# Optimization experiments

Hardware: AMD Instinct MI355X
Metric: run time of the kernel (lower is better)

Reference implementation:

```python
import jax, jax.numpy as jnp
import numpy as np

STRIDE = 1
PAD = 1
DIL = 1


def setup_inputs() -> dict:
    key = jax.random.key(0)
    k1, k2, k3, k4 = jax.random.split(key, 4)
    N, Cin, H, W = 4, 256, 64, 64
    Cout, kh, kw = 256, 3, 3
    inputs = jax.random.normal(k1, (N, Cin, H, W), jnp.float32)
    filter = jax.random.normal(k2, (Cout, Cin, kh, kw), jnp.float32) * 0.05
    # offsets in pixels (y,x interleaved per tap), typical magnitude O(1)
    offset = jax.random.normal(k3, (N, 2 * kh * kw, H, W), jnp.float32)
    # modulation mask in [0,1) (post-sigmoid in real nets)
    mask = jax.random.uniform(k4, (N, kh * kw, H, W), jnp.float32)
    return {"inputs": inputs, "filter": filter, "offset": offset, "mask": mask}


def _dcn_forward(inputs, filt, offset, mask):
    N, C, H, W = inputs.shape
    Cout, _, kh, kw = filt.shape
    K = kh * kw
    Ho = (H + 2 * PAD - DIL * (kh - 1) - 1) // STRIDE + 1
    Wo = (W + 2 * PAD - DIL * (kw - 1) - 1) // STRIDE + 1

    # base sampling grid per kernel tap: [K, Ho, Wo]
    ki, kj = jnp.meshgrid(jnp.arange(kh), jnp.arange(kw), indexing='ij')
    ki = ki.reshape(K, 1, 1)
    kj = kj.reshape(K, 1, 1)
    base_y = (jnp.arange(Ho)[None, :, None] * STRIDE - PAD + ki * DIL).astype(jnp.float32)
    base_x = (jnp.arange(Wo)[None, None, :] * STRIDE - PAD + kj * DIL).astype(jnp.float32)

    # offset channels: per tap k, channel 2k = dy, channel 2k+1 = dx
    off = offset.reshape(N, K, 2, Ho, Wo)
    y = base_y[None] + off[:, :, 0]  # [N, K, Ho, Wo]
    x = base_x[None] + off[:, :, 1]

    y0 = jnp.floor(y)
    x0 = jnp.floor(x)
    ly = y - y0  # fractional parts, [N, K, Ho, Wo]
    lx = x - x0
    y0i = y0.astype(jnp.int32)
    x0i = x0.astype(jnp.int32)

    def gather(img, yy, xx):
        # img [C,H,W]; yy,xx [K,Ho,Wo] int; zero outside bounds
        valid = (yy >= 0) & (yy < H) & (xx >= 0) & (xx < W)
        yc = jnp.clip(yy, 0, H - 1)
        xc = jnp.clip(xx, 0, W - 1)
        return img[:, yc, xc] * valid.astype(img.dtype)  # [C,K,Ho,Wo]

    def sample_one(img, y0i, x0i, ly, lx):
        v00 = gather(img, y0i, x0i)
        v01 = gather(img, y0i, x0i + 1)
        v10 = gather(img, y0i + 1, x0i)
        v11 = gather(img, y0i + 1, x0i + 1)
        return (v00 * (1 - ly) * (1 - lx) + v01 * (1 - ly) * lx
                + v10 * ly * (1 - lx) + v11 * ly * lx)

    # bilinear-sampled, modulated im2col columns: [N, C, K, Ho, Wo]
    col = jax.vmap(sample_one)(inputs, y0i, x0i, ly, lx)
    col = col * mask.reshape(N, 1, K, Ho, Wo)

    # grouped conv with num_groups=1: plain GEMM over (C, K)
    out = jnp.einsum('ock,nckhw->nohw', filt.reshape(Cout, C, K), col)
    return out


def reference(inputs, filter, offset, mask):
    return _dcn_forward(inputs, filter, offset, mask)
```

## Files before the change

kernel.cpp:

```cpp
#include <hip/hip_runtime.h>
#include <stdint.h>

typedef __attribute__((ext_vector_type(4))) float f32x4;
typedef __attribute__((ext_vector_type(8))) short bf16x8;

static constexpr int N_ = 4, C_ = 256, HW_ = 4096;
static constexpr int CO_ = 256, KTAP = 9, KK = 2304;
static constexpr int NSTEP = 72;
static constexpr int A_STEP_BYTES = 16 * 64 * 16;

static constexpr size_t NHWC_BYTES = (size_t)N_ * HW_ * C_ * 2;
static constexpr size_t ABF_OFF    = NHWC_BYTES;
static constexpr size_t ABF_BYTES  = (size_t)NSTEP * A_STEP_BYTES;

__device__ inline unsigned f2bf(float f) {
  unsigned u = __builtin_bit_cast(unsigned, f);
  unsigned r = u + 0x7FFFu + ((u >> 16) & 1u);
  return r >> 16;
}
__device__ inline float asf(unsigned u) { return __builtin_bit_cast(float, u); }

__global__ __launch_bounds__(256) void k_nchw_to_nhwc(const float* __restrict__ in,
                                                      unsigned short* __restrict__ nhwc) {
  __shared__ float tile[64][65];
  int b = blockIdx.x;
  int n = b >> 8, cg = (b >> 6) & 3, hwg = b & 63;
  int c0 = cg * 64, hw0 = hwg * 64;
  int t = threadIdx.x;
  int col = t & 63, r0 = t >> 6;
  const float* src = in + (size_t)(n * C_ + c0) * HW_ + hw0;
#pragma unroll
  for (int i = 0; i < 16; ++i) {
    int row = r0 + i * 4;
    tile[row][col] = src[(size_t)row * HW_ + col];
  }
  __syncthreads();
  int pr = t >> 2, cc0 = (t & 3) * 16;
  unsigned us[8];
#pragma unroll
  for (int i = 0; i < 8; ++i) {
    unsigned lo = f2bf(tile[cc0 + 2 * i][pr]);
    unsigned hi = f2bf(tile[cc0 + 2 * i + 1][pr]);
    us[i] = lo | (hi << 16);
  }
  unsigned* dst = (unsigned*)(nhwc + (size_t)(n * HW_ + hw0 + pr) * C_ + c0 + cc0);
  ((uint4*)dst)[0] = make_uint4(us[0], us[1], us[2], us[3]);
  ((uint4*)dst)[1] = make_uint4(us[4], us[5], us[6], us[7]);
}

__global__ __launch_bounds__(256) void k_prep_filter(const float* __restrict__ filt,
                                                     unsigned short* __restrict__ abf2) {
  int gid = blockIdx.x * 256 + threadIdx.x;
  int o = gid >> 8, c = gid & 255;
  const float* f = filt + (size_t)(o * C_ + c) * KTAP;
  int rb = o >> 4;
  int lane = ((c >> 3) & 3) * 16 + (o & 15);
  int j = c & 7;
#pragma unroll
  for (int tap = 0; tap < KTAP; ++tap) {
    int s = tap * 8 + (c >> 5);
    abf2[((size_t)(s * 16 + rb) * 64 + lane) * 8 + j] = (unsigned short)f2bf(f[tap]);
  }
}

__device__ __forceinline__ void buildB(const uint2* g, f32x4 w, unsigned short* dst) {
  float r0 = w.x * asf(g[0].x << 16) + w.y * asf(g[1].x << 16) +
             w.z * asf(g[2].x << 16) + w.w * asf(g[3].x << 16);
  float r1 = w.x * asf(g[0].x & 0xffff0000u) + w.y * asf(g[1].x & 0xffff0000u) +
             w.z * asf(g[2].x & 0xffff0000u) + w.w * asf(g[3].x & 0xffff0000u);
  float r2 = w.x * asf(g[0].y << 16) + w.y * asf(g[1].y << 16) +
             w.z * asf(g[2].y << 16) + w.w * asf(g[3].y << 16);
  float r3 = w.x * asf(g[0].y & 0xffff0000u) + w.y * asf(g[1].y & 0xffff0000u) +
             w.z * asf(g[2].y & 0xffff0000u) + w.w * asf(g[3].y & 0xffff0000u);
  *(uint2*)dst = make_uint2(f2bf(r0) | (f2bf(r1) << 16), f2bf(r2) | (f2bf(r3) << 16));
}

#define MFMA_BF16 __builtin_amdgcn_mfma_f32_16x16x32_bf16

#define PIPE_STEP(S, GCON, WCON, GISS, WISS, AC0, AC1, AN0, AN1, RDP, WRP)            \
  do {                                                                                \
    int s1_ = (S) + 1; if (s1_ >= NSTEP) s1_ = NSTEP - 1;                             \
    int s2_ = (S) + 2; if (s2_ >= NSTEP) s2_ = NSTEP - 1;                             \
    AN0 = *(const bf16x8*)(aoff0 + (size_t)s1_ * A_STEP_BYTES);                       \
    AN1 = *(const bf16x8*)(aoff1 + (size_t)s1_ * A_STEP_BYTES);                       \
    if ((s2_ & 7) == 0) {                                                             \
      int tp_ = s2_ >> 3;                                                             \
      raS = *(const uint4*)&recA[(tp_ * 64 + p_b) * 4];                               \
      wS  = *(const f32x4*)&recW[(tp_ * 64 + p_b) * 4];                               \
    }                                                                                 \
    {                                                                                 \
      unsigned sc_ = (unsigned)((s2_ & 7) * 64);                                      \
      GISS[0] = *(const uint2*)(nb_t + raS.x + sc_);                                  \
      GISS[1] = *(const uint2*)(nb_t + raS.y + sc_);                                  \
      GISS[2] = *(const uint2*)(nb_t + raS.z + sc_);                                  \
      GISS[3] = *(const uint2*)(nb_t + raS.w + sc_);                                  \
    }                                                                                 \
    WISS = wS;                                                                        \
    __builtin_amdgcn_sched_barrier(0);                                                \
    {                                                                                 \
      const char* bb_ = (const char*)&Bl[RDP][0] + boff;                              \
      bf16x8 b0_ = *(const bf16x8*)(bb_);                                             \
      bf16x8 b1_ = *(const bf16x8*)(bb_ + 1280);                                      \
      bf16x8 b2_ = *(const bf16x8*)(bb_ + 2560);                                      \
      bf16x8 b3_ = *(const bf16x8*)(bb_ + 3840);                                      \
      __builtin_amdgcn_s_setprio(1);                                                  \
      acc[0][0] = MFMA_BF16(AC0, b0_, acc[0][0], 0, 0, 0);                            \
      acc[1][0] = MFMA_BF16(AC1, b0_, acc[1][0], 0, 0, 0);                            \
      acc[0][1] = MFMA_BF16(AC0, b1_, acc[0][1], 0, 0, 0);                            \
      acc[1][1] = MFMA_BF16(AC1, b1_, acc[1][1], 0, 0, 0);                            \
      acc[0][2] = MFMA_BF16(AC0, b2_, acc[0][2], 0, 0, 0);                            \
      acc[1][2] = MFMA_BF16(AC1, b2_, acc[1][2], 0, 0, 0);                            \
      acc[0][3] = MFMA_BF16(AC0, b3_, acc[0][3], 0, 0, 0);                            \
      acc[1][3] = MFMA_BF16(AC1, b3_, acc[1][3], 0, 0, 0);                            \
      __builtin_amdgcn_s_setprio(0);                                                  \
    }                                                                                 \
    buildB(GCON, WCON, (WRP) ? bw1 : bw0);                                            \
    asm volatile("s_waitcnt lgkmcnt(0)" ::: "memory");                                \
    __builtin_amdgcn_s_barrier();                                                     \
    asm volatile("" ::: "memory");                                                    \
  } while (0)

__global__ __launch_bounds__(512, 2) void k_dcn_gemm(const unsigned short* __restrict__ nhwc,
                                                     const unsigned short* __restrict__ abf2,
                                                     const float* __restrict__ offs,
                                                     const float* __restrict__ msk,
                                                     float* __restrict__ out) {
  __shared__ __align__(16) unsigned short Bl[2][64 * 40];
  __shared__ float recW[KTAP * 64 * 4];
  __shared__ unsigned recA[KTAP * 64 * 4];

  int bid = blockIdx.x;
  int b = ((bid & 7) << 5) | (bid >> 3);
  int n = b >> 6;
  int ho = b & 63;
  int hw0 = ho << 6;
  int t = threadIdx.x;

  for (int r = t; r < 576; r += 512) {
    int pl = r / 9;
    int tap = r - pl * 9;
    int hw = hw0 + pl;
    float dy = offs[(size_t)(n * 18 + 2 * tap) * HW_ + hw];
    float dx = offs[(size_t)(n * 18 + 2 * tap + 1) * HW_ + hw];
    float mk = msk[(size_t)(n * 9 + tap) * HW_ + hw];
    float y = (float)(ho - 1 + tap / 3) + dy;
    float x = (float)(pl - 1 + tap % 3) + dx;
    float fy = floorf(y), fx = floorf(x);
    float ly = y - fy, lx = x - fx;
    int y0 = (int)fy, x0 = (int)fx;
    int y1 = y0 + 1, x1 = x0 + 1;
    float vy0 = (y0 >= 0 && y0 < 64) ? 1.f : 0.f;
    float vy1 = (y1 >= 0 && y1 < 64) ? 1.f : 0.f;
    float vx0 = (x0 >= 0 && x0 < 64) ? 1.f : 0.f;
    float vx1 = (x1 >= 0 && x1 < 64) ? 1.f : 0.f;
    int y0c = min(max(y0, 0), 63), y1c = min(max(y1, 0), 63);
    int x0c = min(max(x0, 0), 63), x1c = min(max(x1, 0), 63);
    int base = (tap * 64 + pl) * 4;
    recW[base + 0] = (1.f - ly) * (1.f - lx) * mk * vy0 * vx0;
    recW[base + 1] = (1.f - ly) * lx * mk * vy0 * vx1;
    recW[base + 2] = ly * (1.f - lx) * mk * vy1 * vx0;
    recW[base + 3] = ly * lx * mk * vy1 * vx1;
    recA[base + 0] = (unsigned)((y0c * 64 + x0c) * 512);
    recA[base + 1] = (unsigned)((y0c * 64 + x1c) * 512);
    recA[base + 2] = (unsigned)((y1c * 64 + x0c) * 512);
    recA[base + 3] = (unsigned)((y1c * 64 + x1c) * 512);
  }
  __syncthreads();

  int lane = t & 63, wv = t >> 6;
  int p_b = t >> 3, cg = t & 7;

  const char* aoff0 = (const char*)abf2 + ((wv * 2 + 0) * 64 + lane) * 16;
  const char* aoff1 = (const char*)abf2 + ((wv * 2 + 1) * 64 + lane) * 16;
  const char* nb_t = (const char*)nhwc + (size_t)n * HW_ * C_ * 2 + cg * 8;
  unsigned short* bw0 = &Bl[0][p_b * 40 + cg * 4];
  unsigned short* bw1 = &Bl[1][p_b * 40 + cg * 4];
  const int boff = ((lane & 15) * 40 + (lane >> 4) * 8) * 2;

  f32x4 acc[2][4];
#pragma unroll
  for (int mi = 0; mi < 2; ++mi)
#pragma unroll
    for (int ni = 0; ni < 4; ++ni) acc[mi][ni] = (f32x4){0.f, 0.f, 0.f, 0.f};

  uint2 gA[4], gB[4];
  f32x4 wA, wB, wS;
  uint4 raS;

  raS = *(const uint4*)&recA[p_b * 4];
  wS  = *(const f32x4*)&recW[p_b * 4];
  gA[0] = *(const uint2*)(nb_t + raS.x);
  gA[1] = *(const uint2*)(nb_t + raS.y);
  gA[2] = *(const uint2*)(nb_t + raS.z);
  gA[3] = *(const uint2*)(nb_t + raS.w);
  wA = wS;
  gB[0] = *(const uint2*)(nb_t + raS.x + 64);
  gB[1] = *(const uint2*)(nb_t + raS.y + 64);
  gB[2] = *(const uint2*)(nb_t + raS.z + 64);
  gB[3] = *(const uint2*)(nb_t + raS.w + 64);
  wB = wS;
  bf16x8 afc0 = *(const bf16x8*)(aoff0);
  bf16x8 afc1 = *(const bf16x8*)(aoff1);
  bf16x8 afn0, afn1;

  buildB(gA, wA, bw0);
  asm volatile("s_waitcnt lgkmcnt(0)" ::: "memory");
  __builtin_amdgcn_s_barrier();
  asm volatile("" ::: "memory");

  for (int s = 0; s < NSTEP; s += 2) {
    PIPE_STEP(s,     gB, wB, gA, wA, afc0, afc1, afn0, afn1, 0, 1);
    PIPE_STEP(s + 1, gA, wA, gB, wB, afn0, afn1, afc0, afc1, 1, 0);
  }

  float* ob = out + (size_t)n * CO_ * HW_ + hw0;
#pragma unroll
  for (int mi = 0; mi < 2; ++mi)
#pragma unroll
    for (int ni = 0; ni < 4; ++ni)
#pragma unroll
      for (int j = 0; j < 4; ++j) {
        int o = wv * 32 + mi * 16 + (lane >> 4) * 4 + j;
        int hw = ni * 16 + (lane & 15);
        ob[(size_t)o * HW_ + hw] = acc[mi][ni][j];
      }
}

extern "C" void kernel_launch(void* const* d_in, const int* in_sizes, int n_in,
                              void* d_out, int out_size, void* d_ws, size_t ws_size,
                              hipStream_t stream) {
  const float* inp  = (const float*)d_in[0];
  const float* filt = (const float*)d_in[1];
  const float* offs = (const float*)d_in[2];
  const float* msk  = (const float*)d_in[3];
  float* out = (float*)d_out;
  if (ws_size < ABF_OFF + ABF_BYTES) return;
  unsigned short* nhwc = (unsigned short*)d_ws;
  unsigned short* abf2 = (unsigned short*)((char*)d_ws + ABF_OFF);

  k_nchw_to_nhwc<<<1024, 256, 0, stream>>>(inp, nhwc);
  k_prep_filter<<<256, 256, 0, stream>>>(filt, abf2);
  k_dcn_gemm<<<256, 512, 0, stream>>>(nhwc, abf2, offs, msk, out);
}
```

Baseline: 56.35 us.

## Process two K-steps per barrier phase with a swizzled-free LDS B layout

```diff
diff --git a/kernel.cpp b/kernel.cpp
--- a/kernel.cpp
+++ b/kernel.cpp
@@ -63,7 +63,10 @@
   }
 }
 
-__device__ __forceinline__ void buildB(const uint2* g, f32x4 w, unsigned short* dst) {
+struct GBank { uint2 g[8]; f32x4 w; };
+struct AFrags { bf16x8 f[4]; };
+
+__device__ __forceinline__ void buildB4(const uint2* g, f32x4 w, char* dst) {
   float r0 = w.x * asf(g[0].x << 16) + w.y * asf(g[1].x << 16) +
              w.z * asf(g[2].x << 16) + w.w * asf(g[3].x << 16);
   float r1 = w.x * asf(g[0].x & 0xffff0000u) + w.y * asf(g[1].x & 0xffff0000u) +
@@ -77,47 +80,68 @@
 
 #define MFMA_BF16 __builtin_amdgcn_mfma_f32_16x16x32_bf16
 
-#define PIPE_STEP(S, GCON, WCON, GISS, WISS, AC0, AC1, AN0, AN1, RDP, WRP)            \
-  do {                                                                                \
-    int s1_ = (S) + 1; if (s1_ >= NSTEP) s1_ = NSTEP - 1;                             \
-    int s2_ = (S) + 2; if (s2_ >= NSTEP) s2_ = NSTEP - 1;                             \
-    AN0 = *(const bf16x8*)(aoff0 + (size_t)s1_ * A_STEP_BYTES);                       \
-    AN1 = *(const bf16x8*)(aoff1 + (size_t)s1_ * A_STEP_BYTES);                       \
-    if ((s2_ & 7) == 0) {                                                             \
-      int tp_ = s2_ >> 3;                                                             \
-      raS = *(const uint4*)&recA[(tp_ * 64 + p_b) * 4];                               \
-      wS  = *(const f32x4*)&recW[(tp_ * 64 + p_b) * 4];                               \
-    }                                                                                 \
-    {                                                                                 \
-      unsigned sc_ = (unsigned)((s2_ & 7) * 64);                                      \
-      GISS[0] = *(const uint2*)(nb_t + raS.x + sc_);                                  \
-      GISS[1] = *(const uint2*)(nb_t + raS.y + sc_);                                  \
-      GISS[2] = *(const uint2*)(nb_t + raS.z + sc_);                                  \
-      GISS[3] = *(const uint2*)(nb_t + raS.w + sc_);                                  \
-    }                                                                                 \
-    WISS = wS;                                                                        \
-    __builtin_amdgcn_sched_barrier(0);                                                \
-    {                                                                                 \
-      const char* bb_ = (const char*)&Bl[RDP][0] + boff;                              \
-      bf16x8 b0_ = *(const bf16x8*)(bb_);                                             \
-      bf16x8 b1_ = *(const bf16x8*)(bb_ + 1280);                                      \
-      bf16x8 b2_ = *(const bf16x8*)(bb_ + 2560);                                      \
-      bf16x8 b3_ = *(const bf16x8*)(bb_ + 3840);                                      \
-      __builtin_amdgcn_s_setprio(1);                                                  \
-      acc[0][0] = MFMA_BF16(AC0, b0_, acc[0][0], 0, 0, 0);                            \
-      acc[1][0] = MFMA_BF16(AC1, b0_, acc[1][0], 0, 0, 0);                            \
-      acc[0][1] = MFMA_BF16(AC0, b1_, acc[0][1], 0, 0, 0);                            \
-      acc[1][1] = MFMA_BF16(AC1, b1_, acc[1][1], 0, 0, 0);                            \
-      acc[0][2] = MFMA_BF16(AC0, b2_, acc[0][2], 0, 0, 0);                            \
-      acc[1][2] = MFMA_BF16(AC1, b2_, acc[1][2], 0, 0, 0);                            \
-      acc[0][3] = MFMA_BF16(AC0, b3_, acc[0][3], 0, 0, 0);                            \
-      acc[1][3] = MFMA_BF16(AC1, b3_, acc[1][3], 0, 0, 0);                            \
-      __builtin_amdgcn_s_setprio(0);                                                  \
-    }                                                                                 \
-    buildB(GCON, WCON, (WRP) ? bw1 : bw0);                                            \
-    asm volatile("s_waitcnt lgkmcnt(0)" ::: "memory");                                \
-    __builtin_amdgcn_s_barrier();                                                     \
-    asm volatile("" ::: "memory");                                                    \
+#define PHASE(S, GC, GI, AC, AN, RDP, WRP)                                        \
+  do {                                                                            \
+    int sa_ = (S) + 2 < NSTEP ? (S) + 2 : NSTEP - 1;                              \
+    int sb_ = (S) + 3 < NSTEP ? (S) + 3 : NSTEP - 1;                              \
+    int s4_ = (S) + 4 < NSTEP ? (S) + 4 : NSTEP - 1;                              \
+    int s5_ = (S) + 5 < NSTEP ? (S) + 5 : NSTEP - 1;                              \
+    AN.f[0] = *(const bf16x8*)(aoff0 + (size_t)sa_ * A_STEP_BYTES);               \
+    AN.f[1] = *(const bf16x8*)(aoff1 + (size_t)sa_ * A_STEP_BYTES);               \
+    AN.f[2] = *(const bf16x8*)(aoff0 + (size_t)sb_ * A_STEP_BYTES);               \
+    AN.f[3] = *(const bf16x8*)(aoff1 + (size_t)sb_ * A_STEP_BYTES);               \
+    {                                                                             \
+      int tp_ = s4_ >> 3;                                                         \
+      uint4 ra_ = *(const uint4*)&recA[(tp_ * 64 + p_b) * 4];                     \
+      GI.w = *(const f32x4*)&recW[(tp_ * 64 + p_b) * 4];                          \
+      unsigned c4_ = (unsigned)((s4_ & 7) * 64);                                  \
+      unsigned c5_ = (unsigned)((s5_ & 7) * 64);                                  \
+      GI.g[0] = *(const uint2*)(nb_t + ra_.x + c4_);                              \
+      GI.g[1] = *(const uint2*)(nb_t + ra_.y + c4_);                              \
+      GI.g[2] = *(const uint2*)(nb_t + ra_.z + c4_);                              \
+      GI.g[3] = *(const uint2*)(nb_t + ra_.w + c4_);                              \
+      GI.g[4] = *(const uint2*)(nb_t + ra_.x + c5_);                              \
+      GI.g[5] = *(const uint2*)(nb_t + ra_.y + c5_);                              \
+      GI.g[6] = *(const uint2*)(nb_t + ra_.z + c5_);                              \
+      GI.g[7] = *(const uint2*)(nb_t + ra_.w + c5_);                              \
+    }                                                                             \
+    __builtin_amdgcn_sched_barrier(0);                                            \
+    {                                                                             \
+      const char* bb_ = (const char*)&Bl[0][0] + (RDP) * 8192 + boff;             \
+      bf16x8 b0_ = *(const bf16x8*)(bb_ + 0);                                     \
+      bf16x8 b1_ = *(const bf16x8*)(bb_ + 256);                                   \
+      bf16x8 b2_ = *(const bf16x8*)(bb_ + 512);                                   \
+      bf16x8 b3_ = *(const bf16x8*)(bb_ + 768);                                   \
+      __builtin_amdgcn_s_setprio(1);                                              \
+      acc[0][0] = MFMA_BF16(AC.f[0], b0_, acc[0][0], 0, 0, 0);                    \
+      acc[1][0] = MFMA_BF16(AC.f[1], b0_, acc[1][0], 0, 0, 0);                    \
+      acc[0][1] = MFMA_BF16(AC.f[0], b1_, acc[0][1], 0, 0, 0);                    \
+      acc[1][1] = MFMA_BF16(AC.f[1], b1_, acc[1][1], 0, 0, 0);                    \
+      acc[0][2] = MFMA_BF16(AC.f[0], b2_, acc[0][2], 0, 0, 0);                    \
+      acc[1][2] = MFMA_BF16(AC.f[1], b2_, acc[1][2], 0, 0, 0);                    \
+      acc[0][3] = MFMA_BF16(AC.f[0], b3_, acc[0][3], 0, 0, 0);                    \
+      acc[1][3] = MFMA_BF16(AC.f[1], b3_, acc[1][3], 0, 0, 0);                    \
+      __builtin_amdgcn_s_setprio(0);                                              \
+      bf16x8 b4_ = *(const bf16x8*)(bb_ + 4096 + 0);                              \
+      bf16x8 b5_ = *(const bf16x8*)(bb_ + 4096 + 256);                            \
+      bf16x8 b6_ = *(const bf16x8*)(bb_ + 4096 + 512);                            \
+      bf16x8 b7_ = *(const bf16x8*)(bb_ + 4096 + 768);                            \
+      __builtin_amdgcn_s_setprio(1);                                              \
+      acc[0][0] = MFMA_BF16(AC.f[2], b4_, acc[0][0], 0, 0, 0);                    \
+      acc[1][0] = MFMA_BF16(AC.f[3], b4_, acc[1][0], 0, 0, 0);                    \
+      acc[0][1] = MFMA_BF16(AC.f[2], b5_, acc[0][1], 0, 0, 0);                    \
+      acc[1][1] = MFMA_BF16(AC.f[3], b5_, acc[1][1], 0, 0, 0);                    \
+      acc[0][2] = MFMA_BF16(AC.f[2], b6_, acc[0][2], 0, 0, 0);                    \
+      acc[1][2] = MFMA_BF16(AC.f[3], b6_, acc[1][2], 0, 0, 0);                    \
+      acc[0][3] = MFMA_BF16(AC.f[2], b7_, acc[0][3], 0, 0, 0);                    \
+      acc[1][3] = MFMA_BF16(AC.f[3], b7_, acc[1][3], 0, 0, 0);                    \
+      __builtin_amdgcn_s_setprio(0);                                              \
+    }                                                                             \
+    buildB4(&GC.g[0], GC.w, bwp + (WRP) * 8192 + 0);                              \
+    buildB4(&GC.g[4], GC.w, bwp + (WRP) * 8192 + 4096);                           \
+    asm volatile("s_waitcnt lgkmcnt(0)" ::: "memory");                            \
+    __builtin_amdgcn_s_barrier();                                                 \
+    asm volatile("" ::: "memory");                                                \
   } while (0)
 
 __global__ __launch_bounds__(512, 2) void k_dcn_gemm(const unsigned short* __restrict__ nhwc,
@@ -125,7 +149,7 @@
                                                      const float* __restrict__ offs,
                                                      const float* __restrict__ msk,
                                                      float* __restrict__ out) {
-  __shared__ __align__(16) unsigned short Bl[2][64 * 40];
+  __shared__ __align__(16) unsigned short Bl[2][4096];
   __shared__ float recW[KTAP * 64 * 4];
   __shared__ unsigned recA[KTAP * 64 * 4];
 
@@ -173,9 +197,8 @@
   const char* aoff0 = (const char*)abf2 + ((wv * 2 + 0) * 64 + lane) * 16;
   const char* aoff1 = (const char*)abf2 + ((wv * 2 + 1) * 64 + lane) * 16;
   const char* nb_t = (const char*)nhwc + (size_t)n * HW_ * C_ * 2 + cg * 8;
-  unsigned short* bw0 = &Bl[0][p_b * 40 + cg * 4];
-  unsigned short* bw1 = &Bl[1][p_b * 40 + cg * 4];
-  const int boff = ((lane & 15) * 40 + (lane >> 4) * 8) * 2;
+  char* bwp = (char*)&Bl[0][0] + ((cg >> 1) * 1024 + p_b * 16 + (cg & 1) * 8);
+  const int boff = (lane >> 4) * 1024 + (lane & 15) * 16;
 
   f32x4 acc[2][4];
 #pragma unroll
@@ -183,34 +206,44 @@
 #pragma unroll
     for (int ni = 0; ni < 4; ++ni) acc[mi][ni] = (f32x4){0.f, 0.f, 0.f, 0.f};
 
-  uint2 gA[4], gB[4];
-  f32x4 wA, wB, wS;
-  uint4 raS;
-
-  raS = *(const uint4*)&recA[p_b * 4];
-  wS  = *(const f32x4*)&recW[p_b * 4];
-  gA[0] = *(const uint2*)(nb_t + raS.x);
-  gA[1] = *(const uint2*)(nb_t + raS.y);
-  gA[2] = *(const uint2*)(nb_t + raS.z);
-  gA[3] = *(const uint2*)(nb_t + raS.w);
-  wA = wS;
-  gB[0] = *(const uint2*)(nb_t + raS.x + 64);
-  gB[1] = *(const uint2*)(nb_t + raS.y + 64);
-  gB[2] = *(const uint2*)(nb_t + raS.z + 64);
-  gB[3] = *(const uint2*)(nb_t + raS.w + 64);
-  wB = wS;
-  bf16x8 afc0 = *(const bf16x8*)(aoff0);
-  bf16x8 afc1 = *(const bf16x8*)(aoff1);
-  bf16x8 afn0, afn1;
-
-  buildB(gA, wA, bw0);
-  asm volatile("s_waitcnt lgkmcnt(0)" ::: "memory");
-  __builtin_amdgcn_s_barrier();
-  asm volatile("" ::: "memory");
-
-  for (int s = 0; s < NSTEP; s += 2) {
-    PIPE_STEP(s,     gB, wB, gA, wA, afc0, afc1, afn0, afn1, 0, 1);
-    PIPE_STEP(s + 1, gA, wA, gB, wB, afn0, afn1, afc0, afc1, 1, 0);
+  GBank gA, gB;
+  AFrags aC, aN;
+
+  {
+    uint4 ra0 = *(const uint4*)&recA[p_b * 4];
+    f32x4 w0 = *(const f32x4*)&recW[p_b * 4];
+    gA.w = w0;
+    gB.w = w0;
+    gA.g[0] = *(const uint2*)(nb_t + ra0.x + 0);
+    gA.g[1] = *(const uint2*)(nb_t + ra0.y + 0);
+    gA.g[2] = *(const uint2*)(nb_t + ra0.z + 0);
+    gA.g[3] = *(const uint2*)(nb_t + ra0.w + 0);
+    gA.g[4] = *(const uint2*)(nb_t + ra0.x + 64);
+    gA.g[5] = *(const uint2*)(nb_t + ra0.y + 64);
+    gA.g[6] = *(const uint2*)(nb_t + ra0.z + 64);
+    gA.g[7] = *(const uint2*)(nb_t + ra0.w + 64);
+    gB.g[0] = *(const uint2*)(nb_t + ra0.x + 128);
+    gB.g[1] = *(const uint2*)(nb_t + ra0.y + 128);
+    gB.g[2] = *(const uint2*)(nb_t + ra0.z + 128);
+    gB.g[3] = *(const uint2*)(nb_t + ra0.w + 128);
+    gB.g[4] = *(const uint2*)(nb_t + ra0.x + 192);
+    gB.g[5] = *(const uint2*)(nb_t + ra0.y + 192);
+    gB.g[6] = *(const uint2*)(nb_t + ra0.z + 192);
+    gB.g[7] = *(const uint2*)(nb_t + ra0.w + 192);
+    aC.f[0] = *(const bf16x8*)(aoff0);
+    aC.f[1] = *(const bf16x8*)(aoff1);
+    aC.f[2] = *(const bf16x8*)(aoff0 + A_STEP_BYTES);
+    aC.f[3] = *(const bf16x8*)(aoff1 + A_STEP_BYTES);
+    buildB4(&gA.g[0], gA.w, bwp + 0);
+    buildB4(&gA.g[4], gA.w, bwp + 4096);
+    asm volatile("s_waitcnt lgkmcnt(0)" ::: "memory");
+    __builtin_amdgcn_s_barrier();
+    asm volatile("" ::: "memory");
+  }
+
+  for (int s = 0; s < NSTEP; s += 4) {
+    PHASE(s,     gB, gA, aC, aN, 0, 1);
+    PHASE(s + 2, gA, gB, aN, aC, 1, 0);
   }
 
   float* ob = out + (size_t)n * CO_ * HW_ + hw0;
```

Measured after the change: 59.78 us. +6.1%, slower.

## Double threads per block, halve per-wave work, swizzle B tile layout

Applied to the files above, without the earlier changes.

```diff
diff --git a/kernel.cpp b/kernel.cpp
--- a/kernel.cpp
+++ b/kernel.cpp
@@ -63,69 +63,62 @@
   }
 }
 
-__device__ __forceinline__ void buildB(const uint2* g, f32x4 w, unsigned short* dst) {
-  float r0 = w.x * asf(g[0].x << 16) + w.y * asf(g[1].x << 16) +
-             w.z * asf(g[2].x << 16) + w.w * asf(g[3].x << 16);
-  float r1 = w.x * asf(g[0].x & 0xffff0000u) + w.y * asf(g[1].x & 0xffff0000u) +
-             w.z * asf(g[2].x & 0xffff0000u) + w.w * asf(g[3].x & 0xffff0000u);
-  float r2 = w.x * asf(g[0].y << 16) + w.y * asf(g[1].y << 16) +
-             w.z * asf(g[2].y << 16) + w.w * asf(g[3].y << 16);
-  float r3 = w.x * asf(g[0].y & 0xffff0000u) + w.y * asf(g[1].y & 0xffff0000u) +
-             w.z * asf(g[2].y & 0xffff0000u) + w.w * asf(g[3].y & 0xffff0000u);
-  *(uint2*)dst = make_uint2(f2bf(r0) | (f2bf(r1) << 16), f2bf(r2) | (f2bf(r3) << 16));
+struct GB { unsigned g[4]; f32x4 w; };
+
+__device__ __forceinline__ void buildB2(const unsigned* g, f32x4 w, char* dst) {
+  float r0 = w.x * asf(g[0] << 16) + w.y * asf(g[1] << 16) +
+             w.z * asf(g[2] << 16) + w.w * asf(g[3] << 16);
+  float r1 = w.x * asf(g[0] & 0xffff0000u) + w.y * asf(g[1] & 0xffff0000u) +
+             w.z * asf(g[2] & 0xffff0000u) + w.w * asf(g[3] & 0xffff0000u);
+  *(unsigned*)dst = f2bf(r0) | (f2bf(r1) << 16);
 }
 
 #define MFMA_BF16 __builtin_amdgcn_mfma_f32_16x16x32_bf16
 
-#define PIPE_STEP(S, GCON, WCON, GISS, WISS, AC0, AC1, AN0, AN1, RDP, WRP)            \
-  do {                                                                                \
-    int s1_ = (S) + 1; if (s1_ >= NSTEP) s1_ = NSTEP - 1;                             \
-    int s2_ = (S) + 2; if (s2_ >= NSTEP) s2_ = NSTEP - 1;                             \
-    AN0 = *(const bf16x8*)(aoff0 + (size_t)s1_ * A_STEP_BYTES);                       \
-    AN1 = *(const bf16x8*)(aoff1 + (size_t)s1_ * A_STEP_BYTES);                       \
-    if ((s2_ & 7) == 0) {                                                             \
-      int tp_ = s2_ >> 3;                                                             \
-      raS = *(const uint4*)&recA[(tp_ * 64 + p_b) * 4];                               \
-      wS  = *(const f32x4*)&recW[(tp_ * 64 + p_b) * 4];                               \
-    }                                                                                 \
-    {                                                                                 \
-      unsigned sc_ = (unsigned)((s2_ & 7) * 64);                                      \
-      GISS[0] = *(const uint2*)(nb_t + raS.x + sc_);                                  \
-      GISS[1] = *(const uint2*)(nb_t + raS.y + sc_);                                  \
-      GISS[2] = *(const uint2*)(nb_t + raS.z + sc_);                                  \
-      GISS[3] = *(const uint2*)(nb_t + raS.w + sc_);                                  \
-    }                                                                                 \
-    WISS = wS;                                                                        \
-    __builtin_amdgcn_sched_barrier(0);                                                \
-    {                                                                                 \
-      const char* bb_ = (const char*)&Bl[RDP][0] + boff;                              \
-      bf16x8 b0_ = *(const bf16x8*)(bb_);                                             \
-      bf16x8 b1_ = *(const bf16x8*)(bb_ + 1280);                                      \
-      bf16x8 b2_ = *(const bf16x8*)(bb_ + 2560);                                      \
-      bf16x8 b3_ = *(const bf16x8*)(bb_ + 3840);                                      \
-      __builtin_amdgcn_s_setprio(1);                                                  \
-      acc[0][0] = MFMA_BF16(AC0, b0_, acc[0][0], 0, 0, 0);                            \
-      acc[1][0] = MFMA_BF16(AC1, b0_, acc[1][0], 0, 0, 0);                            \
-      acc[0][1] = MFMA_BF16(AC0, b1_, acc[0][1], 0, 0, 0);                            \
-      acc[1][1] = MFMA_BF16(AC1, b1_, acc[1][1], 0, 0, 0);                            \
-      acc[0][2] = MFMA_BF16(AC0, b2_, acc[0][2], 0, 0, 0);                            \
-      acc[1][2] = MFMA_BF16(AC1, b2_, acc[1][2], 0, 0, 0);                            \
-      acc[0][3] = MFMA_BF16(AC0, b3_, acc[0][3], 0, 0, 0);                            \
-      acc[1][3] = MFMA_BF16(AC1, b3_, acc[1][3], 0, 0, 0);                            \
-      __builtin_amdgcn_s_setprio(0);                                                  \
-    }                                                                                 \
-    buildB(GCON, WCON, (WRP) ? bw1 : bw0);                                            \
-    asm volatile("s_waitcnt lgkmcnt(0)" ::: "memory");                                \
-    __builtin_amdgcn_s_barrier();                                                     \
-    asm volatile("" ::: "memory");                                                    \
+#define PIPE(S, GCON, GISS, ACUR, ANXT, RDP, WRP)                                 \
+  do {                                                                            \
+    int s1_ = (S) + 1 < NSTEP ? (S) + 1 : NSTEP - 1;                              \
+    int s2_ = (S) + 2 < NSTEP ? (S) + 2 : NSTEP - 1;                              \
+    ANXT = *(const bf16x8*)(aoff + (size_t)s1_ * A_STEP_BYTES);                   \
+    if ((s2_ & 7) == 0) {                                                         \
+      int tp_ = s2_ >> 3;                                                         \
+      raS = *(const uint4*)&recA[(tp_ * 64 + p_b) * 4];                           \
+      wS  = *(const f32x4*)&recW[(tp_ * 64 + p_b) * 4];                           \
+    }                                                                             \
+    {                                                                             \
+      unsigned co_ = (unsigned)((s2_ & 7) * 64);                                  \
+      GISS.g[0] = *(const unsigned*)(nb_t + raS.x + co_);                         \
+      GISS.g[1] = *(const unsigned*)(nb_t + raS.y + co_);                         \
+      GISS.g[2] = *(const unsigned*)(nb_t + raS.z + co_);                         \
+      GISS.g[3] = *(const unsigned*)(nb_t + raS.w + co_);                         \
+      GISS.w = wS;                                                                \
+    }                                                                             \
+    __builtin_amdgcn_sched_barrier(0);                                            \
+    {                                                                             \
+      const char* bb_ = (const char*)&Bl[0][0] + (RDP) * 4096;                    \
+      bf16x8 b0_ = *(const bf16x8*)(bb_ + bo0);                                   \
+      bf16x8 b1_ = *(const bf16x8*)(bb_ + bo1);                                   \
+      bf16x8 b2_ = *(const bf16x8*)(bb_ + bo2);                                   \
+      bf16x8 b3_ = *(const bf16x8*)(bb_ + bo3);                                   \
+      __builtin_amdgcn_s_setprio(1);                                              \
+      acc[0] = MFMA_BF16(ACUR, b0_, acc[0], 0, 0, 0);                             \
+      acc[1] = MFMA_BF16(ACUR, b1_, acc[1], 0, 0, 0);                             \
+      acc[2] = MFMA_BF16(ACUR, b2_, acc[2], 0, 0, 0);                             \
+      acc[3] = MFMA_BF16(ACUR, b3_, acc[3], 0, 0, 0);                             \
+      __builtin_amdgcn_s_setprio(0);                                              \
+    }                                                                             \
+    buildB2(GCON.g, GCON.w, (WRP) ? bw1 : bw0);                                   \
+    asm volatile("s_waitcnt lgkmcnt(0)" ::: "memory");                            \
+    __builtin_amdgcn_s_barrier();                                                 \
+    asm volatile("" ::: "memory");                                                \
   } while (0)
 
-__global__ __launch_bounds__(512, 2) void k_dcn_gemm(const unsigned short* __restrict__ nhwc,
-                                                     const unsigned short* __restrict__ abf2,
-                                                     const float* __restrict__ offs,
-                                                     const float* __restrict__ msk,
-                                                     float* __restrict__ out) {
-  __shared__ __align__(16) unsigned short Bl[2][64 * 40];
+__global__ __launch_bounds__(1024, 4) void k_dcn_gemm(const unsigned short* __restrict__ nhwc,
+                                                      const unsigned short* __restrict__ abf2,
+                                                      const float* __restrict__ offs,
+                                                      const float* __restrict__ msk,
+                                                      float* __restrict__ out) {
+  __shared__ __align__(16) unsigned short Bl[2][2048];
   __shared__ float recW[KTAP * 64 * 4];
   __shared__ unsigned recA[KTAP * 64 * 4];
 
@@ -136,7 +129,7 @@
   int hw0 = ho << 6;
   int t = threadIdx.x;
 
-  for (int r = t; r < 576; r += 512) {
+  for (int r = t; r < 576; r += 1024) {
     int pl = r / 9;
     int tap = r - pl * 9;
     int hw = hw0 + pl;
@@ -168,62 +161,64 @@
   __syncthreads();
 
   int lane = t & 63, wv = t >> 6;
-  int p_b = t >> 3, cg = t & 7;
-
-  const char* aoff0 = (const char*)abf2 + ((wv * 2 + 0) * 64 + lane) * 16;
-  const char* aoff1 = (const char*)abf2 + ((wv * 2 + 1) * 64 + lane) * 16;
-  const char* nb_t = (const char*)nhwc + (size_t)n * HW_ * C_ * 2 + cg * 8;
-  unsigned short* bw0 = &Bl[0][p_b * 40 + cg * 4];
-  unsigned short* bw1 = &Bl[1][p_b * 40 + cg * 4];
-  const int boff = ((lane & 15) * 40 + (lane >> 4) * 8) * 2;
-
-  f32x4 acc[2][4];
-#pragma unroll
-  for (int mi = 0; mi < 2; ++mi)
-#pragma unroll
-    for (int ni = 0; ni < 4; ++ni) acc[mi][ni] = (f32x4){0.f, 0.f, 0.f, 0.f};
-
-  uint2 gA[4], gB[4];
-  f32x4 wA, wB, wS;
+  int p_b = t >> 4;
+  int cg = t & 15;
+  int cq = cg >> 2, ck = cg & 3;
+
+  const char* aoff = (const char*)abf2 + ((size_t)(wv * 64 + lane)) * 16;
+  const char* nb_t = (const char*)nhwc + (size_t)n * HW_ * C_ * 2 + cg * 4;
+  int wbyte = cq * 1024 + (((p_b + 4 * cq) & 63) * 16) + ck * 4;
+  char* bw0 = (char*)&Bl[0][0] + wbyte;
+  char* bw1 = (char*)&Bl[0][0] + 4096 + wbyte;
+
+  int cqr = lane >> 4;
+  int rslot = (lane & 15) + 4 * cqr;
+  const int bo0 = cqr * 1024 + ((rslot + 0) & 63) * 16;
+  const int bo1 = cqr * 1024 + ((rslot + 16) & 63) * 16;
+  const int bo2 = cqr * 1024 + ((rslot + 32) & 63) * 16;
+  const int bo3 = cqr * 1024 + ((rslot + 48) & 63) * 16;
+
+  f32x4 acc[4];
+#pragma unroll
+  for (int ni = 0; ni < 4; ++ni) acc[ni] = (f32x4){0.f, 0.f, 0.f, 0.f};
+
+  GB gA, gB;
+  bf16x8 afc, afn;
   uint4 raS;
+  f32x4 wS;
 
   raS = *(const uint4*)&recA[p_b * 4];
   wS  = *(const f32x4*)&recW[p_b * 4];
-  gA[0] = *(const uint2*)(nb_t + raS.x);
-  gA[1] = *(const uint2*)(nb_t + raS.y);
-  gA[2] = *(const uint2*)(nb_t + raS.z);
-  gA[3] = *(const uint2*)(nb_t + raS.w);
-  wA = wS;
-  gB[0] = *(const uint2*)(nb_t + raS.x + 64);
-  gB[1] = *(const uint2*)(nb_t + raS.y + 64);
-  gB[2] = *(const uint2*)(nb_t + raS.z + 64);
-  gB[3] = *(const uint2*)(nb_t + raS.w + 64);
-  wB = wS;
-  bf16x8 afc0 = *(const bf16x8*)(aoff0);
-  bf16x8 afc1 = *(const bf16x8*)(aoff1);
-  bf16x8 afn0, afn1;
-
-  buildB(gA, wA, bw0);
+  gA.g[0] = *(const unsigned*)(nb_t + raS.x);
+  gA.g[1] = *(const unsigned*)(nb_t + raS.y);
+  gA.g[2] = *(const unsigned*)(nb_t + raS.z);
+  gA.g[3] = *(const unsigned*)(nb_t + raS.w);
+  gA.w = wS;
+  gB.g[0] = *(const unsigned*)(nb_t + raS.x + 64);
+  gB.g[1] = *(const unsigned*)(nb_t + raS.y + 64);
+  gB.g[2] = *(const unsigned*)(nb_t + raS.z + 64);
+  gB.g[3] = *(const unsigned*)(nb_t + raS.w + 64);
+  gB.w = wS;
+  afc = *(const bf16x8*)(aoff);
+  buildB2(gA.g, gA.w, bw0);
   asm volatile("s_waitcnt lgkmcnt(0)" ::: "memory");
   __builtin_amdgcn_s_barrier();
   asm volatile("" ::: "memory");
 
   for (int s = 0; s < NSTEP; s += 2) {
-    PIPE_STEP(s,     gB, wB, gA, wA, afc0, afc1, afn0, afn1, 0, 1);
-    PIPE_STEP(s + 1, gA, wA, gB, wB, afn0, afn1, afc0, afc1, 1, 0);
+    PIPE(s,     gB, gA, afc, afn, 0, 1);
+    PIPE(s + 1, gA, gB, afn, afc, 1, 0);
   }
 
   float* ob = out + (size_t)n * CO_ * HW_ + hw0;
 #pragma unroll
-  for (int mi = 0; mi < 2; ++mi)
-#pragma unroll
-    for (int ni = 0; ni < 4; ++ni)
-#pragma unroll
-      for (int j = 0; j < 4; ++j) {
-        int o = wv * 32 + mi * 16 + (lane >> 4) * 4 + j;
-        int hw = ni * 16 + (lane & 15);
-        ob[(size_t)o * HW_ + hw] = acc[mi][ni][j];
-      }
+  for (int ni = 0; ni < 4; ++ni)
+#pragma unroll
+    for (int j = 0; j < 4; ++j) {
+      int o = wv * 16 + (lane >> 4) * 4 + j;
+      int hw = ni * 16 + (lane & 15);
+      ob[(size_t)o * HW_ + hw] = acc[ni][j];
+    }
 }
 
 extern "C" void kernel_launch(void* const* d_in, const int* in_sizes, int n_in,
@@ -240,5 +235,5 @@
 
   k_nchw_to_nhwc<<<1024, 256, 0, stream>>>(inp, nhwc);
   k_prep_filter<<<256, 256, 0, stream>>>(filt, abf2);
-  k_dcn_gemm<<<256, 512, 0, stream>>>(nhwc, abf2, offs, msk, out);
-}
+  k_dcn_gemm<<<256, 1024, 0, stream>>>(nhwc, abf2, offs, msk, out);
+}
```

After: 56.48 us. About the same (+0.2%).
